# Kernel optimization log

Measured on AMD Instinct MI355X. Metric: run time of the kernel, lower is better.

The kernel has to match this reference:

```python
import jax, jax.numpy as jnp
import numpy as np

CLASS_NUM = 8
OUT_SIZE = 160
EPS = 1e-8


def conv1x1(x, w, b):
    # x: [B,Cin,H,W], w: [Cout,Cin], b: [Cout]
    return jnp.einsum('oc,bchw->bohw', w, x) + b[None, :, None, None]


def setup_inputs() -> dict:
    key = jax.random.key(0)
    ks = jax.random.split(key, 8)
    Cin, Cout = 256, 128
    B, H, W = 16, 80, 80
    feature = jax.random.normal(ks[0], (B, Cin, H, W), dtype=jnp.float32)
    fusion_label = jax.random.randint(ks[1], (B, 1, OUT_SIZE, OUT_SIZE), 0, CLASS_NUM, dtype=jnp.int64) if jax.config.jax_enable_x64 else jax.random.randint(ks[1], (B, 1, OUT_SIZE, OUT_SIZE), 0, CLASS_NUM).astype(jnp.int32)
    w1 = jax.random.normal(ks[2], (2 * Cin, Cin), dtype=jnp.float32) * 0.05
    b1 = jnp.zeros((2 * Cin,), dtype=jnp.float32)
    w2 = jax.random.normal(ks[3], (Cin, 2 * Cin), dtype=jnp.float32) * 0.05
    b2 = jnp.zeros((Cin,), dtype=jnp.float32)
    w3 = jax.random.normal(ks[4], (Cout, Cin), dtype=jnp.float32) * 0.05
    b3 = jnp.zeros((Cout,), dtype=jnp.float32)
    return {"feature": feature, "fusion_label": fusion_label,
            "w1": w1, "b1": b1, "w2": w2, "b2": b2, "w3": w3, "b3": b3}


def reference(feature, fusion_label, w1, b1, w2, b2, w3, b3):
    # 1x1 conv stack with ReLUs (conv1 in the torch module)
    f = jax.nn.relu(conv1x1(feature, w1, b1))
    f = jax.nn.relu(conv1x1(f, w2, b2))
    f2 = jax.nn.relu(conv1x1(f, w3, b3))
    B, C = f2.shape[0], f2.shape[1]
    # bilinear resize, half-pixel centers == torch align_corners=False
    f3 = jax.image.resize(f2, (B, C, OUT_SIZE, OUT_SIZE), method='bilinear', antialias=False)
    # per-class masked mean pooling (segment mean over spatial positions)
    lbl = fusion_label[:, 0]  # [B,H,W]
    onehot = jax.nn.one_hot(lbl, CLASS_NUM, dtype=f3.dtype)  # [B,H,W,K]
    counts = onehot.sum((1, 2))  # [B,K]
    pooled = jnp.einsum('bhwk,bchw->bkc', onehot, f3) / (counts + EPS)[..., None]
    presence = (counts > 0).astype(jnp.int32)  # which (image, class) rows the torch code would emit
    return pooled, presence
```

## Files before the change

### kernel.cpp

```cpp
#include <hip/hip_runtime.h>

#define B_SZ   16
#define P_IN   6400
#define H_IN   80
#define OUTHW  160
#define NCLASS 8

typedef __attribute__((ext_vector_type(8))) short  short8v;
typedef __attribute__((ext_vector_type(4))) float  f32x4;
typedef __attribute__((ext_vector_type(4))) unsigned short ushort4v;

__device__ __forceinline__ unsigned short f2bf(float x) {
    union { float f; unsigned int u; } v; v.f = x;
    unsigned int r = v.u + 0x7fffu + ((v.u >> 16) & 1u);
    return (unsigned short)(r >> 16);
}
__device__ __forceinline__ float bf2f(unsigned short h) {
    union { unsigned int u; float f; } v; v.u = ((unsigned int)h) << 16;
    return v.f;
}

__device__ __forceinline__ void gload16(const void* g, void* lds) {
    __builtin_amdgcn_global_load_lds(
        (const __attribute__((address_space(1))) unsigned int*)g,
        (__attribute__((address_space(3))) unsigned int*)lds, 16, 0, 0);
}

__global__ void wprep3(const float* __restrict__ w1, const float* __restrict__ w2,
                       const float* __restrict__ w3,
                       unsigned short* __restrict__ h1, unsigned short* __restrict__ l1,
                       unsigned short* __restrict__ h2, unsigned short* __restrict__ l2,
                       unsigned short* __restrict__ h3, unsigned short* __restrict__ l3)
{
    int i = blockIdx.x * 256 + threadIdx.x;
    const float* src; unsigned short *h, *l; int off;
    if (i < 131072)      { src = w1; h = h1; l = l1; off = i; }
    else if (i < 262144) { src = w2; h = h2; l = l2; off = i - 131072; }
    else                 { src = w3; h = h3; l = l3; off = i - 262144;
                           if (off >= 32768) return; }
    float v = src[off];
    unsigned short hi = f2bf(v);
    h[off] = hi;
    l[off] = f2bf(v - bf2f(hi));
}

__global__ __launch_bounds__(256, 2)
void conv1_fused(const unsigned short* __restrict__ Wh, const unsigned short* __restrict__ Wl,
                 const float* __restrict__ bias,
                 const float* __restrict__ F,
                 unsigned short* __restrict__ Y)
{
    constexpr int K = 256, NK = 8, NM = 4, M = 512;
    __shared__ unsigned short As_h[2][4096], As_l[2][4096];
    __shared__ float Bf[2][4096];
    const int tid = threadIdx.x, lane = tid & 63, w = tid >> 6;
    const int wm = w >> 1, wn = w & 1;

    const int nb = gridDim.x, id = blockIdx.x;
    const int wg = (id & 7) * (nb >> 3) + (id >> 3);
    const int bb  = wg / (50 * NM);
    const int rem = wg - bb * (50 * NM);
    const int n0 = (rem / NM) * 128;
    const int m0 = (rem - (rem / NM) * NM) * NM == 0 ? (rem % NM) * 128 : (rem % NM) * 128;

    const size_t abase = (size_t)m0 * K;
    const size_t fbase = (size_t)bb * 256 * P_IN + n0;

    f32x4 acc[4][4];
#pragma unroll
    for (int i = 0; i < 4; ++i)
#pragma unroll
        for (int j = 0; j < 4; ++j) acc[i][j] = (f32x4)0.f;

    int a_row[2], a_k8[2], a_lo[2];
#pragma unroll
    for (int q = 0; q < 2; ++q) {
        const int ch = 2 * w + q;
        a_row[q] = ch * 16 + (lane >> 2);
        a_k8[q]  = ((((lane & 3) - (a_row[q] >> 1)) & 3) << 3);
        a_lo[q]  = ch * 512;
    }
    int b_k[4], b_src[4], b_lo[4];
#pragma unroll
    for (int q = 0; q < 4; ++q) {
        b_k[q]   = q * 8 + w * 2 + (lane >> 5);
        const int inrow = (lane & 31) * 4;
        b_src[q] = inrow ^ ((((b_k[q] >> 3) & 1)) << 4);
        b_lo[q]  = q * 1024 + w * 256 + lane * 4;
    }
    const int gsel = lane >> 4;
    int off_a[4], bidx[4];
#pragma unroll
    for (int mi = 0; mi < 4; ++mi) {
        const int r = wm * 64 + mi * 16 + (lane & 15);
        off_a[mi] = r * 32 + (((gsel + (r >> 1)) & 3) << 3);
    }
#pragma unroll
    for (int ni = 0; ni < 4; ++ni) {
        const int nl = wn * 64 + ni * 16 + (lane & 15);
        bidx[ni] = ((gsel * 8) * 128 + nl) ^ ((gsel & 1) << 4);
    }

#define STAGE1(buf, kt) do {                                                  \
    _Pragma("unroll")                                                         \
    for (int q = 0; q < 4; ++q) {                                             \
        const size_t gx = fbase + (size_t)((kt) * 32 + b_k[q]) * P_IN + b_src[q]; \
        gload16(F + gx, &Bf[buf][b_lo[q]]);                                   \
    }                                                                         \
    _Pragma("unroll")                                                         \
    for (int q = 0; q < 2; ++q) {                                             \
        const size_t gW = abase + (size_t)a_row[q] * K + (kt) * 32 + a_k8[q]; \
        gload16(Wh + gW, &As_h[buf][a_lo[q]]);                                \
        gload16(Wl + gW, &As_l[buf][a_lo[q]]);                                \
    }                                                                         \
} while (0)

    int cur = 0;
    STAGE1(0, 0);
    __syncthreads();

    for (int t = 0; t < NK; ++t) {
        if (t + 1 < NK) {
            STAGE1(cur ^ 1, t + 1);
            asm volatile("s_waitcnt vmcnt(8)" ::: "memory");
        } else {
            asm volatile("s_waitcnt vmcnt(0)" ::: "memory");
        }
        __builtin_amdgcn_s_barrier();
        __builtin_amdgcn_sched_barrier(0);

        short8v ah[4], al[4], bv[4];
#pragma unroll
        for (int mi = 0; mi < 4; ++mi) {
            ah[mi] = *(const short8v*)&As_h[cur][off_a[mi]];
            al[mi] = *(const short8v*)&As_l[cur][off_a[mi]];
        }
#pragma unroll
        for (int ni = 0; ni < 4; ++ni) {
            union { short8v v; unsigned short u[8]; } pk;
#pragma unroll
            for (int j = 0; j < 8; ++j)
                pk.u[j] = f2bf(Bf[cur][bidx[ni] + j * 128]);
            bv[ni] = pk.v;
        }
#pragma unroll
        for (int mi = 0; mi < 4; ++mi)
#pragma unroll
            for (int ni = 0; ni < 4; ++ni) {
                acc[mi][ni] = __builtin_amdgcn_mfma_f32_16x16x32_bf16(ah[mi], bv[ni], acc[mi][ni], 0, 0, 0);
                acc[mi][ni] = __builtin_amdgcn_mfma_f32_16x16x32_bf16(al[mi], bv[ni], acc[mi][ni], 0, 0, 0);
            }
        asm volatile("s_waitcnt lgkmcnt(0)" ::: "memory");
        __builtin_amdgcn_sched_barrier(0);
        __builtin_amdgcn_s_barrier();
        cur ^= 1;
    }
#undef STAGE1

    const int lhi = lane >> 4;
#pragma unroll
    for (int mi = 0; mi < 4; ++mi) {
        const int m_base = m0 + wm * 64 + mi * 16 + lhi * 4;
        const float4 b4 = *(const float4*)&bias[m_base];
#pragma unroll
        for (int ni = 0; ni < 4; ++ni) {
            const int n = n0 + wn * 64 + ni * 16 + (lane & 15);
            const size_t o = ((size_t)bb * P_IN + n) * M + m_base;
            ushort4v u;
            u.x = f2bf(fmaxf(acc[mi][ni][0] + b4.x, 0.f));
            u.y = f2bf(fmaxf(acc[mi][ni][1] + b4.y, 0.f));
            u.z = f2bf(fmaxf(acc[mi][ni][2] + b4.z, 0.f));
            u.w = f2bf(fmaxf(acc[mi][ni][3] + b4.w, 0.f));
            *(ushort4v*)&Y[o] = u;
        }
    }
}

template<int K, int NM>
__global__ __launch_bounds__(256, 3)
void conv_mfma(const unsigned short* __restrict__ Wh, const unsigned short* __restrict__ Wl,
               const float* __restrict__ bias,
               const unsigned short* __restrict__ X, unsigned short* __restrict__ Y)
{
    constexpr int M  = NM * 128;
    constexpr int NK = K / 32;
    __shared__ unsigned short As_h[2][4096], As_l[2][4096], Bs[2][4096];
    const int tid = threadIdx.x, lane = tid & 63, w = tid >> 6;
    const int wm = w >> 1, wn = w & 1;

    const int nb = gridDim.x, id = blockIdx.x;
    const int wg = (id & 7) * (nb >> 3) + (id >> 3);
    const int bb  = wg / (50 * NM);
    const int rem = wg - bb * (50 * NM);
    const int n0 = (rem / NM) * 128;
    const int m0 = (rem % NM) * 128;

    const size_t abase = (size_t)m0 * K;
    const size_t xbase = ((size_t)bb * P_IN + n0) * K;

    f32x4 acc[4][4];
#pragma unroll
    for (int i = 0; i < 4; ++i)
#pragma unroll
        for (int j = 0; j < 4; ++j) acc[i][j] = (f32x4)0.f;

    int s_row[2], s_k8[2], s_lo[2];
#pragma unroll
    for (int q = 0; q < 2; ++q) {
        const int ch = 2 * w + q;
        s_row[q] = ch * 16 + (lane >> 2);
        s_k8[q]  = ((((lane & 3) - (s_row[q] >> 1)) & 3) << 3);
        s_lo[q]  = ch * 512;
    }
    int off_a[4], off_b[4];
    const int gsel = lane >> 4;
#pragma unroll
    for (int mi = 0; mi < 4; ++mi) {
        const int r = wm * 64 + mi * 16 + (lane & 15);
        off_a[mi] = r * 32 + (((gsel + (r >> 1)) & 3) << 3);
    }
#pragma unroll
    for (int ni = 0; ni < 4; ++ni) {
        const int r = wn * 64 + ni * 16 + (lane & 15);
        off_b[ni] = r * 32 + (((gsel + (r >> 1)) & 3) << 3);
    }

#define STAGE(buf, kt) do {                                                   \
    _Pragma("unroll")                                                         \
    for (int q = 0; q < 2; ++q) {                                             \
        const size_t kof = (size_t)(kt) * 32 + s_k8[q];                       \
        const size_t gW  = abase + (size_t)s_row[q] * K + kof;                \
        const size_t gX  = xbase + (size_t)s_row[q] * K + kof;                \
        gload16(Wh + gW, &As_h[buf][s_lo[q]]);                                \
        gload16(Wl + gW, &As_l[buf][s_lo[q]]);                                \
        gload16(X  + gX, &Bs[buf][s_lo[q]]);                                  \
    }                                                                         \
} while (0)

    int cur = 0;
    STAGE(0, 0);
    __syncthreads();

    for (int t = 0; t < NK; ++t) {
        if (t + 1 < NK) {
            STAGE(cur ^ 1, t + 1);
            asm volatile("s_waitcnt vmcnt(6)" ::: "memory");
        } else {
            asm volatile("s_waitcnt vmcnt(0)" ::: "memory");
        }
        __builtin_amdgcn_s_barrier();
        __builtin_amdgcn_sched_barrier(0);

        short8v ah[4], al[4], bv[4];
#pragma unroll
        for (int mi = 0; mi < 4; ++mi) {
            ah[mi] = *(const short8v*)&As_h[cur][off_a[mi]];
            al[mi] = *(const short8v*)&As_l[cur][off_a[mi]];
        }
#pragma unroll
        for (int ni = 0; ni < 4; ++ni)
            bv[ni] = *(const short8v*)&Bs[cur][off_b[ni]];
#pragma unroll
        for (int mi = 0; mi < 4; ++mi)
#pragma unroll
            for (int ni = 0; ni < 4; ++ni) {
                acc[mi][ni] = __builtin_amdgcn_mfma_f32_16x16x32_bf16(ah[mi], bv[ni], acc[mi][ni], 0, 0, 0);
                acc[mi][ni] = __builtin_amdgcn_mfma_f32_16x16x32_bf16(al[mi], bv[ni], acc[mi][ni], 0, 0, 0);
            }
        asm volatile("s_waitcnt lgkmcnt(0)" ::: "memory");
        __builtin_amdgcn_sched_barrier(0);
        __builtin_amdgcn_s_barrier();
        cur ^= 1;
    }
#undef STAGE

    const int lhi = lane >> 4;
#pragma unroll
    for (int mi = 0; mi < 4; ++mi) {
        const int m_base = m0 + wm * 64 + mi * 16 + lhi * 4;
        const float4 b4 = *(const float4*)&bias[m_base];
#pragma unroll
        for (int ni = 0; ni < 4; ++ni) {
            const int n = n0 + wn * 64 + ni * 16 + (lane & 15);
            const size_t o = ((size_t)bb * P_IN + n) * M + m_base;
            ushort4v u;
            u.x = f2bf(fmaxf(acc[mi][ni][0] + b4.x, 0.f));
            u.y = f2bf(fmaxf(acc[mi][ni][1] + b4.y, 0.f));
            u.z = f2bf(fmaxf(acc[mi][ni][2] + b4.z, 0.f));
            u.w = f2bf(fmaxf(acc[mi][ni][3] + b4.w, 0.f));
            *(ushort4v*)&Y[o] = u;
        }
    }
}

__global__ __launch_bounds__(256)
void label_scatter(const int* __restrict__ lbl, float* __restrict__ g,
                   float* __restrict__ counts)
{
    __shared__ float sg[NCLASS][8][80];
    __shared__ float hist[NCLASS];
    const int b = blockIdx.x, slab = blockIdx.y;
    const int tid = threadIdx.x;
    const int r0 = slab * 8;
    for (int i = tid; i < NCLASS * 8 * 80; i += 256) ((float*)sg)[i] = 0.f;
    if (tid < NCLASS) hist[tid] = 0.f;
    __syncthreads();

    const int ibase = 2 * r0 - 1;
    for (int idx = tid; idx < 18 * 160; idx += 256) {
        const int ir = idx / 160, j = idx - ir * 160;
        const int i = ibase + ir;
        if (i < 0 || i >= OUTHW) continue;
        const int k = lbl[(size_t)b * (OUTHW * OUTHW) + i * OUTHW + j];
        const int mi = i >> 1, mj = j >> 1;
        int y0, y1, x0, x1; float wy0, wy1, wx0, wx1;
        if (i & 1) { y0 = mi; y1 = (mi < H_IN - 1) ? mi + 1 : H_IN - 1; wy0 = 0.75f; wy1 = 0.25f; }
        else       { y0 = (mi > 0) ? mi - 1 : 0; y1 = mi;               wy0 = 0.25f; wy1 = 0.75f; }
        if (j & 1) { x0 = mj; x1 = (mj < H_IN - 1) ? mj + 1 : H_IN - 1; wx0 = 0.75f; wx1 = 0.25f; }
        else       { x0 = (mj > 0) ? mj - 1 : 0; x1 = mj;               wx0 = 0.25f; wx1 = 0.75f; }
        if (mi >= r0 && mi < r0 + 8) atomicAdd(&hist[k], 1.f);
        const int ry0 = y0 - r0, ry1 = y1 - r0;
        if (ry0 >= 0 && ry0 < 8) {
            atomicAdd(&sg[k][ry0][x0], wy0 * wx0);
            atomicAdd(&sg[k][ry0][x1], wy0 * wx1);
        }
        if (ry1 >= 0 && ry1 < 8) {
            atomicAdd(&sg[k][ry1][x0], wy1 * wx0);
            atomicAdd(&sg[k][ry1][x1], wy1 * wx1);
        }
    }
    __syncthreads();
    for (int i = tid; i < NCLASS * 8 * 80; i += 256) {
        const int k = i / 640, rem2 = i - k * 640;
        g[((size_t)b * NCLASS + k) * P_IN + r0 * 80 + rem2] = ((const float*)sg)[i];
    }
    if (tid < NCLASS) atomicAdd(&counts[b * NCLASS + tid], hist[tid]);
}

__global__ __launch_bounds__(256)
void pool2(const unsigned short* __restrict__ f3, const float* __restrict__ g,
           float* __restrict__ pooled)
{
    __shared__ float sg[NCLASS][800];
    const int b = blockIdx.x, chunk = blockIdx.y;
    const int tid = threadIdx.x;
#pragma unroll
    for (int i = 0; i < 25; ++i) {
        int idx = i * 256 + tid;
        int k = idx / 800, p = idx - k * 800;
        sg[k][p] = g[((size_t)b * NCLASS + k) * P_IN + chunk * 800 + p];
    }
    __syncthreads();

    const int c  = tid & 127;
    const int kg = tid >> 7;
    float acc0 = 0.f, acc1 = 0.f, acc2 = 0.f, acc3 = 0.f;
    const unsigned short* fb = f3 + ((size_t)b * P_IN + chunk * 800) * 128 + c;
    for (int p = 0; p < 800; ++p) {
        const float fv = bf2f(fb[(size_t)p * 128]);
        acc0 = fmaf(fv, sg[kg * 4 + 0][p], acc0);
        acc1 = fmaf(fv, sg[kg * 4 + 1][p], acc1);
        acc2 = fmaf(fv, sg[kg * 4 + 2][p], acc2);
        acc3 = fmaf(fv, sg[kg * 4 + 3][p], acc3);
    }
    atomicAdd(&pooled[((size_t)b * NCLASS + kg * 4 + 0) * 128 + c], acc0);
    atomicAdd(&pooled[((size_t)b * NCLASS + kg * 4 + 1) * 128 + c], acc1);
    atomicAdd(&pooled[((size_t)b * NCLASS + kg * 4 + 2) * 128 + c], acc2);
    atomicAdd(&pooled[((size_t)b * NCLASS + kg * 4 + 3) * 128 + c], acc3);
}

__global__ void finalize(const float* __restrict__ pooled, const float* __restrict__ counts,
                         float* __restrict__ out)
{
    const int b = blockIdx.x;
#pragma unroll
    for (int i = threadIdx.x; i < NCLASS * 128; i += 256) {
        const int k = i >> 7;
        const float cnt = counts[b * NCLASS + k];
        out[(size_t)b * NCLASS * 128 + i] = pooled[(size_t)b * NCLASS * 128 + i] / (cnt + 1e-8f);
    }
    if (threadIdx.x < NCLASS)
        out[B_SZ * NCLASS * 128 + b * NCLASS + threadIdx.x] =
            (counts[b * NCLASS + threadIdx.x] > 0.f) ? 1.f : 0.f;
}

extern "C" void kernel_launch(void* const* d_in, const int* in_sizes, int n_in,
                              void* d_out, int out_size, void* d_ws, size_t ws_size,
                              hipStream_t stream)
{
    const float* feature = (const float*)d_in[0];
    const int*   lbl     = (const int*)d_in[1];
    const float* w1 = (const float*)d_in[2];
    const float* b1 = (const float*)d_in[3];
    const float* w2 = (const float*)d_in[4];
    const float* b2 = (const float*)d_in[5];
    const float* w3 = (const float*)d_in[6];
    const float* b3 = (const float*)d_in[7];
    float* out = (float*)d_out;

    char* ws = (char*)d_ws;
    unsigned short* f1  = (unsigned short*)(ws);
    unsigned short* f2  = (unsigned short*)(ws + 104857600);
    unsigned short* f3  = (unsigned short*)(ws + 157286400);
    unsigned short* Wh1 = (unsigned short*)(ws + 183500800);
    unsigned short* Wl1 = (unsigned short*)(ws + 183762944);
    unsigned short* Wh2 = (unsigned short*)(ws + 184025088);
    unsigned short* Wl2 = (unsigned short*)(ws + 184287232);
    unsigned short* Wh3 = (unsigned short*)(ws + 184549376);
    unsigned short* Wl3 = (unsigned short*)(ws + 184614912);
    float* g      = (float*)(ws + 184680448);
    float* counts = (float*)(ws + 187957248);
    float* pooled = (float*)(ws + 187957760);

    hipMemsetAsync(counts, 0, 512 + 65536, stream);

    wprep3<<<1152, 256, 0, stream>>>(w1, w2, w3, Wh1, Wl1, Wh2, Wl2, Wh3, Wl3);

    conv1_fused<<<3200, 256, 0, stream>>>(Wh1, Wl1, b1, feature, f1);
    conv_mfma<512, 2><<<1600, 256, 0, stream>>>(Wh2, Wl2, b2, f1, f2);
    conv_mfma<256, 1><<<800,  256, 0, stream>>>(Wh3, Wl3, b3, f2, f3);

    label_scatter<<<dim3(B_SZ, 10), 256, 0, stream>>>(lbl, g, counts);
    pool2<<<dim3(B_SZ, 8), 256, 0, stream>>>(f3, g, pooled);
    finalize<<<B_SZ, 256, 0, stream>>>(pooled, counts, out);
}
```

Measured before the change: 404.4 us.

## Convert conv1 input to bf16 in LDS, restage conv_mfma K loop, fuse scatter with pooling

conv1 now loads fp32 feature values into registers, converts them to bf16 once and stores them swizzled in LDS, so each B fragment is read with a single vector load instead of eight scalar fp32 loads plus conversions. Its LDS footprint shrinks and launch bounds are raised to 3 blocks per SM. conv_mfma drops double buffering in favour of 64-wide K steps with an XOR swizzle and a barrier on each side. label_scatter and pool2 are fused so the g scatter buffer no longer goes through global memory. The single-buffered conv_mfma loses load/compute overlap, and the higher occupancy target may cause register spills.

```diff
diff --git a/kernel.cpp b/kernel.cpp
--- a/kernel.cpp
+++ b/kernel.cpp
@@ -44,15 +44,14 @@
     l[off] = f2bf(v - bf2f(hi));
 }
 
-__global__ __launch_bounds__(256, 2)
+__global__ __launch_bounds__(256, 3)
 void conv1_fused(const unsigned short* __restrict__ Wh, const unsigned short* __restrict__ Wl,
                  const float* __restrict__ bias,
                  const float* __restrict__ F,
                  unsigned short* __restrict__ Y)
 {
     constexpr int K = 256, NK = 8, NM = 4, M = 512;
-    __shared__ unsigned short As_h[2][4096], As_l[2][4096];
-    __shared__ float Bf[2][4096];
+    __shared__ unsigned short As_h[2][4096], As_l[2][4096], Bs[2][4096];
     const int tid = threadIdx.x, lane = tid & 63, w = tid >> 6;
     const int wm = w >> 1, wn = w & 1;
 
@@ -61,10 +60,13 @@
     const int bb  = wg / (50 * NM);
     const int rem = wg - bb * (50 * NM);
     const int n0 = (rem / NM) * 128;
-    const int m0 = (rem - (rem / NM) * NM) * NM == 0 ? (rem % NM) * 128 : (rem % NM) * 128;
+    const int m0 = (rem % NM) * 128;
 
     const size_t abase = (size_t)m0 * K;
-    const size_t fbase = (size_t)bb * 256 * P_IN + n0;
+
+    const int bn  = tid & 127;
+    const int bkh = tid >> 7;
+    const float* Fb = F + (size_t)bb * K * P_IN + (size_t)(bkh * 16) * P_IN + n0 + bn;
 
     f32x4 acc[4][4];
 #pragma unroll
@@ -80,16 +82,15 @@
         a_k8[q]  = ((((lane & 3) - (a_row[q] >> 1)) & 3) << 3);
         a_lo[q]  = ch * 512;
     }
-    int b_k[4], b_src[4], b_lo[4];
-#pragma unroll
-    for (int q = 0; q < 4; ++q) {
-        b_k[q]   = q * 8 + w * 2 + (lane >> 5);
-        const int inrow = (lane & 31) * 4;
-        b_src[q] = inrow ^ ((((b_k[q] >> 3) & 1)) << 4);
-        b_lo[q]  = q * 1024 + w * 256 + lane * 4;
+    const int fbn = (bn >> 1) + (bn >> 3);
+    int b_wo[2];
+#pragma unroll
+    for (int h = 0; h < 2; ++h) {
+        const int c = bkh * 2 + h;
+        b_wo[h] = bn * 32 + (((c + fbn) & 3) << 3);
     }
     const int gsel = lane >> 4;
-    int off_a[4], bidx[4];
+    int off_a[4], off_b[4];
 #pragma unroll
     for (int mi = 0; mi < 4; ++mi) {
         const int r = wm * 64 + mi * 16 + (lane & 15);
@@ -97,16 +98,29 @@
     }
 #pragma unroll
     for (int ni = 0; ni < 4; ++ni) {
-        const int nl = wn * 64 + ni * 16 + (lane & 15);
-        bidx[ni] = ((gsel * 8) * 128 + nl) ^ ((gsel & 1) << 4);
-    }
-
-#define STAGE1(buf, kt) do {                                                  \
+        const int r = wn * 64 + ni * 16 + (lane & 15);
+        off_b[ni] = r * 32 + (((gsel + (r >> 1) + (r >> 3)) & 3) << 3);
+    }
+
+    float bld[16];
+
+#define ISSUE_B(kt) do {                                                      \
     _Pragma("unroll")                                                         \
-    for (int q = 0; q < 4; ++q) {                                             \
-        const size_t gx = fbase + (size_t)((kt) * 32 + b_k[q]) * P_IN + b_src[q]; \
-        gload16(F + gx, &Bf[buf][b_lo[q]]);                                   \
+    for (int j = 0; j < 16; ++j)                                              \
+        bld[j] = Fb[(size_t)((kt) * 32 + j) * P_IN];                          \
+} while (0)
+
+#define WRITE_B(buf) do {                                                     \
+    _Pragma("unroll")                                                         \
+    for (int h = 0; h < 2; ++h) {                                             \
+        union { short8v v; unsigned short u[8]; } pk;                         \
+        _Pragma("unroll")                                                     \
+        for (int j = 0; j < 8; ++j) pk.u[j] = f2bf(bld[h * 8 + j]);           \
+        *(short8v*)&Bs[buf][b_wo[h]] = pk.v;                                  \
     }                                                                         \
+} while (0)
+
+#define STAGE_A(buf, kt) do {                                                 \
     _Pragma("unroll")                                                         \
     for (int q = 0; q < 2; ++q) {                                             \
         const size_t gW = abase + (size_t)a_row[q] * K + (kt) * 32 + a_k8[q]; \
@@ -115,20 +129,14 @@
     }                                                                         \
 } while (0)
 
+    ISSUE_B(0);
+    STAGE_A(0, 0);
+    WRITE_B(0);
+    __syncthreads();
+
     int cur = 0;
-    STAGE1(0, 0);
-    __syncthreads();
-
     for (int t = 0; t < NK; ++t) {
-        if (t + 1 < NK) {
-            STAGE1(cur ^ 1, t + 1);
-            asm volatile("s_waitcnt vmcnt(8)" ::: "memory");
-        } else {
-            asm volatile("s_waitcnt vmcnt(0)" ::: "memory");
-        }
-        __builtin_amdgcn_s_barrier();
-        __builtin_amdgcn_sched_barrier(0);
-
+        if (t + 1 < NK) { ISSUE_B(t + 1); STAGE_A(cur ^ 1, t + 1); }
         short8v ah[4], al[4], bv[4];
 #pragma unroll
         for (int mi = 0; mi < 4; ++mi) {
@@ -136,13 +144,8 @@
             al[mi] = *(const short8v*)&As_l[cur][off_a[mi]];
         }
 #pragma unroll
-        for (int ni = 0; ni < 4; ++ni) {
-            union { short8v v; unsigned short u[8]; } pk;
-#pragma unroll
-            for (int j = 0; j < 8; ++j)
-                pk.u[j] = f2bf(Bf[cur][bidx[ni] + j * 128]);
-            bv[ni] = pk.v;
-        }
+        for (int ni = 0; ni < 4; ++ni)
+            bv[ni] = *(const short8v*)&Bs[cur][off_b[ni]];
 #pragma unroll
         for (int mi = 0; mi < 4; ++mi)
 #pragma unroll
@@ -150,12 +153,16 @@
                 acc[mi][ni] = __builtin_amdgcn_mfma_f32_16x16x32_bf16(ah[mi], bv[ni], acc[mi][ni], 0, 0, 0);
                 acc[mi][ni] = __builtin_amdgcn_mfma_f32_16x16x32_bf16(al[mi], bv[ni], acc[mi][ni], 0, 0, 0);
             }
-        asm volatile("s_waitcnt lgkmcnt(0)" ::: "memory");
-        __builtin_amdgcn_sched_barrier(0);
-        __builtin_amdgcn_s_barrier();
+        if (t + 1 < NK) {
+            __builtin_amdgcn_sched_barrier(0);
+            WRITE_B(cur ^ 1);
+        }
+        __syncthreads();
         cur ^= 1;
     }
-#undef STAGE1
+#undef ISSUE_B
+#undef WRITE_B
+#undef STAGE_A
 
     const int lhi = lane >> 4;
 #pragma unroll
@@ -182,9 +189,8 @@
                const float* __restrict__ bias,
                const unsigned short* __restrict__ X, unsigned short* __restrict__ Y)
 {
-    constexpr int M  = NM * 128;
-    constexpr int NK = K / 32;
-    __shared__ unsigned short As_h[2][4096], As_l[2][4096], Bs[2][4096];
+    constexpr int M = NM * 128;
+    __shared__ unsigned short As_h[8192], As_l[8192], Bs[8192];
     const int tid = threadIdx.x, lane = tid & 63, w = tid >> 6;
     const int wm = w >> 1, wn = w & 1;
 
@@ -195,7 +201,6 @@
     const int n0 = (rem / NM) * 128;
     const int m0 = (rem % NM) * 128;
 
-    const size_t abase = (size_t)m0 * K;
     const size_t xbase = ((size_t)bb * P_IN + n0) * K;
 
     f32x4 acc[4][4];
@@ -204,75 +209,50 @@
 #pragma unroll
         for (int j = 0; j < 4; ++j) acc[i][j] = (f32x4)0.f;
 
-    int s_row[2], s_k8[2], s_lo[2];
-#pragma unroll
-    for (int q = 0; q < 2; ++q) {
-        const int ch = 2 * w + q;
-        s_row[q] = ch * 16 + (lane >> 2);
-        s_k8[q]  = ((((lane & 3) - (s_row[q] >> 1)) & 3) << 3);
-        s_lo[q]  = ch * 512;
-    }
-    int off_a[4], off_b[4];
-    const int gsel = lane >> 4;
-#pragma unroll
-    for (int mi = 0; mi < 4; ++mi) {
-        const int r = wm * 64 + mi * 16 + (lane & 15);
-        off_a[mi] = r * 32 + (((gsel + (r >> 1)) & 3) << 3);
-    }
-#pragma unroll
-    for (int ni = 0; ni < 4; ++ni) {
-        const int r = wn * 64 + ni * 16 + (lane & 15);
-        off_b[ni] = r * 32 + (((gsel + (r >> 1)) & 3) << 3);
-    }
-
-#define STAGE(buf, kt) do {                                                   \
-    _Pragma("unroll")                                                         \
-    for (int q = 0; q < 2; ++q) {                                             \
-        const size_t kof = (size_t)(kt) * 32 + s_k8[q];                       \
-        const size_t gW  = abase + (size_t)s_row[q] * K + kof;                \
-        const size_t gX  = xbase + (size_t)s_row[q] * K + kof;                \
-        gload16(Wh + gW, &As_h[buf][s_lo[q]]);                                \
-        gload16(Wl + gW, &As_l[buf][s_lo[q]]);                                \
-        gload16(X  + gX, &Bs[buf][s_lo[q]]);                                  \
-    }                                                                         \
-} while (0)
-
-    int cur = 0;
-    STAGE(0, 0);
-    __syncthreads();
-
-    for (int t = 0; t < NK; ++t) {
-        if (t + 1 < NK) {
-            STAGE(cur ^ 1, t + 1);
-            asm volatile("s_waitcnt vmcnt(6)" ::: "memory");
-        } else {
-            asm volatile("s_waitcnt vmcnt(0)" ::: "memory");
-        }
-        __builtin_amdgcn_s_barrier();
-        __builtin_amdgcn_sched_barrier(0);
-
-        short8v ah[4], al[4], bv[4];
-#pragma unroll
-        for (int mi = 0; mi < 4; ++mi) {
-            ah[mi] = *(const short8v*)&As_h[cur][off_a[mi]];
-            al[mi] = *(const short8v*)&As_l[cur][off_a[mi]];
-        }
-#pragma unroll
-        for (int ni = 0; ni < 4; ++ni)
-            bv[ni] = *(const short8v*)&Bs[cur][off_b[ni]];
-#pragma unroll
-        for (int mi = 0; mi < 4; ++mi)
+    const int srow = lane >> 3;
+    const int scol = lane & 7;
+
+    for (int k0 = 0; k0 < K; k0 += 64) {
+#pragma unroll
+        for (int q = 0; q < 4; ++q) {
+            const int c   = w * 4 + q;
+            const int row = c * 8 + srow;
+            const int kc  = scol ^ (row & 7);
+            const size_t ga = (size_t)(m0 + row) * K + k0 + kc * 8;
+            const size_t gx = xbase + (size_t)row * K + k0 + kc * 8;
+            const int lo = c * 512;
+            gload16(Wh + ga, &As_h[lo]);
+            gload16(Wl + ga, &As_l[lo]);
+            gload16(X + gx, &Bs[lo]);
+        }
+        __syncthreads();
+#pragma unroll
+        for (int s = 0; s < 2; ++s) {
+            short8v ah[4], al[4], bv[4];
+            const int kc = s * 4 + (lane >> 4);
+#pragma unroll
+            for (int mi = 0; mi < 4; ++mi) {
+                const int m = wm * 64 + mi * 16 + (lane & 15);
+                const int off = m * 64 + ((kc ^ (m & 7)) << 3);
+                ah[mi] = *(const short8v*)&As_h[off];
+                al[mi] = *(const short8v*)&As_l[off];
+            }
 #pragma unroll
             for (int ni = 0; ni < 4; ++ni) {
-                acc[mi][ni] = __builtin_amdgcn_mfma_f32_16x16x32_bf16(ah[mi], bv[ni], acc[mi][ni], 0, 0, 0);
-                acc[mi][ni] = __builtin_amdgcn_mfma_f32_16x16x32_bf16(al[mi], bv[ni], acc[mi][ni], 0, 0, 0);
+                const int n = wn * 64 + ni * 16 + (lane & 15);
+                const int off = n * 64 + ((kc ^ (n & 7)) << 3);
+                bv[ni] = *(const short8v*)&Bs[off];
             }
-        asm volatile("s_waitcnt lgkmcnt(0)" ::: "memory");
-        __builtin_amdgcn_sched_barrier(0);
-        __builtin_amdgcn_s_barrier();
-        cur ^= 1;
-    }
-#undef STAGE
+#pragma unroll
+            for (int mi = 0; mi < 4; ++mi)
+#pragma unroll
+                for (int ni = 0; ni < 4; ++ni) {
+                    acc[mi][ni] = __builtin_amdgcn_mfma_f32_16x16x32_bf16(ah[mi], bv[ni], acc[mi][ni], 0, 0, 0);
+                    acc[mi][ni] = __builtin_amdgcn_mfma_f32_16x16x32_bf16(al[mi], bv[ni], acc[mi][ni], 0, 0, 0);
+                }
+        }
+        __syncthreads();
+    }
 
     const int lhi = lane >> 4;
 #pragma unroll
@@ -294,15 +274,15 @@
 }
 
 __global__ __launch_bounds__(256)
-void label_scatter(const int* __restrict__ lbl, float* __restrict__ g,
-                   float* __restrict__ counts)
-{
-    __shared__ float sg[NCLASS][8][80];
+void scatter_pool(const int* __restrict__ lbl, const unsigned short* __restrict__ f3,
+                  float* __restrict__ pooled, float* __restrict__ counts)
+{
+    __shared__ float sg[NCLASS][640];
     __shared__ float hist[NCLASS];
     const int b = blockIdx.x, slab = blockIdx.y;
     const int tid = threadIdx.x;
     const int r0 = slab * 8;
-    for (int i = tid; i < NCLASS * 8 * 80; i += 256) ((float*)sg)[i] = 0.f;
+    for (int i = tid; i < NCLASS * 640; i += 256) ((float*)sg)[i] = 0.f;
     if (tid < NCLASS) hist[tid] = 0.f;
     __syncthreads();
 
@@ -321,42 +301,21 @@
         if (mi >= r0 && mi < r0 + 8) atomicAdd(&hist[k], 1.f);
         const int ry0 = y0 - r0, ry1 = y1 - r0;
         if (ry0 >= 0 && ry0 < 8) {
-            atomicAdd(&sg[k][ry0][x0], wy0 * wx0);
-            atomicAdd(&sg[k][ry0][x1], wy0 * wx1);
+            atomicAdd(&sg[k][ry0 * 80 + x0], wy0 * wx0);
+            atomicAdd(&sg[k][ry0 * 80 + x1], wy0 * wx1);
         }
         if (ry1 >= 0 && ry1 < 8) {
-            atomicAdd(&sg[k][ry1][x0], wy1 * wx0);
-            atomicAdd(&sg[k][ry1][x1], wy1 * wx1);
-        }
-    }
-    __syncthreads();
-    for (int i = tid; i < NCLASS * 8 * 80; i += 256) {
-        const int k = i / 640, rem2 = i - k * 640;
-        g[((size_t)b * NCLASS + k) * P_IN + r0 * 80 + rem2] = ((const float*)sg)[i];
-    }
-    if (tid < NCLASS) atomicAdd(&counts[b * NCLASS + tid], hist[tid]);
-}
-
-__global__ __launch_bounds__(256)
-void pool2(const unsigned short* __restrict__ f3, const float* __restrict__ g,
-           float* __restrict__ pooled)
-{
-    __shared__ float sg[NCLASS][800];
-    const int b = blockIdx.x, chunk = blockIdx.y;
-    const int tid = threadIdx.x;
-#pragma unroll
-    for (int i = 0; i < 25; ++i) {
-        int idx = i * 256 + tid;
-        int k = idx / 800, p = idx - k * 800;
-        sg[k][p] = g[((size_t)b * NCLASS + k) * P_IN + chunk * 800 + p];
+            atomicAdd(&sg[k][ry1 * 80 + x0], wy1 * wx0);
+            atomicAdd(&sg[k][ry1 * 80 + x1], wy1 * wx1);
+        }
     }
     __syncthreads();
 
     const int c  = tid & 127;
     const int kg = tid >> 7;
     float acc0 = 0.f, acc1 = 0.f, acc2 = 0.f, acc3 = 0.f;
-    const unsigned short* fb = f3 + ((size_t)b * P_IN + chunk * 800) * 128 + c;
-    for (int p = 0; p < 800; ++p) {
+    const unsigned short* fb = f3 + ((size_t)b * P_IN + r0 * 80) * 128 + c;
+    for (int p = 0; p < 640; ++p) {
         const float fv = bf2f(fb[(size_t)p * 128]);
         acc0 = fmaf(fv, sg[kg * 4 + 0][p], acc0);
         acc1 = fmaf(fv, sg[kg * 4 + 1][p], acc1);
@@ -367,6 +326,7 @@
     atomicAdd(&pooled[((size_t)b * NCLASS + kg * 4 + 1) * 128 + c], acc1);
     atomicAdd(&pooled[((size_t)b * NCLASS + kg * 4 + 2) * 128 + c], acc2);
     atomicAdd(&pooled[((size_t)b * NCLASS + kg * 4 + 3) * 128 + c], acc3);
+    if (tid < NCLASS) atomicAdd(&counts[b * NCLASS + tid], hist[tid]);
 }
 
 __global__ void finalize(const float* __restrict__ pooled, const float* __restrict__ counts,
@@ -408,9 +368,8 @@
     unsigned short* Wl2 = (unsigned short*)(ws + 184287232);
     unsigned short* Wh3 = (unsigned short*)(ws + 184549376);
     unsigned short* Wl3 = (unsigned short*)(ws + 184614912);
-    float* g      = (float*)(ws + 184680448);
-    float* counts = (float*)(ws + 187957248);
-    float* pooled = (float*)(ws + 187957760);
+    float* counts = (float*)(ws + 184680448);
+    float* pooled = (float*)(ws + 184680960);
 
     hipMemsetAsync(counts, 0, 512 + 65536, stream);
 
@@ -420,7 +379,6 @@
     conv_mfma<512, 2><<<1600, 256, 0, stream>>>(Wh2, Wl2, b2, f1, f2);
     conv_mfma<256, 1><<<800,  256, 0, stream>>>(Wh3, Wl3, b3, f2, f3);
 
-    label_scatter<<<dim3(B_SZ, 10), 256, 0, stream>>>(lbl, g, counts);
-    pool2<<<dim3(B_SZ, 8), 256, 0, stream>>>(f3, g, pooled);
+    scatter_pool<<<dim3(B_SZ, 10), 256, 0, stream>>>(lbl, f3, pooled, counts);
     finalize<<<B_SZ, 256, 0, stream>>>(pooled, counts, out);
 }
```

New measurement: 362.5 us. -10.4%, faster.
